# Kernel tuning notes

Hardware: AMD Instinct MI355X
Metric: run time of the kernel (lower is better)

The kernel has to match this reference:

```python
import jax, jax.numpy as jnp
import numpy as np

B, T, D, H = 2, 2048, 1024, 16  # batch, seq_len, d_model (d_in==d_out), num_heads
HD = D // H  # head_dim = 64


def setup_inputs() -> dict:
    key = jax.random.key(0)
    ks = jax.random.split(key, 6)
    s = 1.0 / np.sqrt(D)
    return {
        "x": jax.random.normal(ks[0], (B, T, D), dtype=jnp.float32),
        "wq": jax.random.normal(ks[1], (D, D), dtype=jnp.float32) * s,
        "wk": jax.random.normal(ks[2], (D, D), dtype=jnp.float32) * s,
        "wv": jax.random.normal(ks[3], (D, D), dtype=jnp.float32) * s,
        "wo": jax.random.normal(ks[4], (D, D), dtype=jnp.float32) * s,
        "bo": jax.random.normal(ks[5], (D,), dtype=jnp.float32) * 0.01,
    }


def reference(x, wq, wk, wv, wo, bo):
    b, t, d = x.shape
    # projections (qkv_bias=False), split heads: [b, h, t, hd]
    q = (x @ wq).reshape(b, t, H, HD).transpose(0, 2, 1, 3)
    k = (x @ wk).reshape(b, t, H, HD).transpose(0, 2, 1, 3)
    v = (x @ wv).reshape(b, t, H, HD).transpose(0, 2, 1, 3)
    # causal attention scores [b, h, t, t]
    scores = jnp.einsum("bhqd,bhkd->bhqk", q, k) / jnp.sqrt(jnp.float32(HD))
    causal = jnp.tril(jnp.ones((t, t), dtype=bool))
    scores = jnp.where(causal[None, None, :, :], scores, -jnp.inf)
    attn = jax.nn.softmax(scores, axis=-1)  # dropout p=0.0 -> identity
    ctx = jnp.einsum("bhqk,bhkd->bhqd", attn, v)  # [b, h, t, hd]
    ctx = ctx.transpose(0, 2, 1, 3).reshape(b, t, d)  # merge heads
    return ctx @ wo + bo
```

## Files before the change

### kernel.cpp

```cpp
#include <hip/hip_runtime.h>
#include <hip/hip_bf16.h>
#include <stdint.h>

#define B_  2
#define T_  2048
#define D_  1024
#define H_  16
#define HD_ 64

typedef __bf16 bf16x8 __attribute__((ext_vector_type(8)));
typedef __bf16 bf16x4 __attribute__((ext_vector_type(4)));
typedef float  f32x4  __attribute__((ext_vector_type(4)));

__device__ __forceinline__ void async_copy16(const void* g, void* l) {
  __builtin_amdgcn_global_load_lds((__attribute__((address_space(1))) void*)(g),
                                   (__attribute__((address_space(3))) void*)(l),
                                   16, 0, 0);
}

__global__ void prep_kernel(const float* __restrict__ x,
                            const float* __restrict__ wq, const float* __restrict__ wk,
                            const float* __restrict__ wv, const float* __restrict__ wo,
                            __bf16* __restrict__ xc,
                            __bf16* __restrict__ wqkv_t, __bf16* __restrict__ wo_t) {
  const int id  = blockIdx.x;
  const int tid = threadIdx.x;
  if (id < 4096) {
    __shared__ __bf16 tile[32][33];
    const int z   = id >> 10;
    const int rem = id & 1023;
    const int n0 = (rem & 31) * 32, k0 = (rem >> 5) * 32;
    const int tx = tid & 31, ty = tid >> 5;
    const float* src = (z == 0) ? wq : (z == 1) ? wk : (z == 2) ? wv : wo;
    __bf16* dst = (z < 3) ? (wqkv_t + (size_t)z * 1024 * 1024) : wo_t;
#pragma unroll
    for (int i = 0; i < 4; ++i)
      tile[ty + 8 * i][tx] = (__bf16)src[(size_t)(k0 + ty + 8 * i) * 1024 + n0 + tx];
    __syncthreads();
#pragma unroll
    for (int i = 0; i < 4; ++i)
      dst[(size_t)(n0 + ty + 8 * i) * 1024 + k0 + tx] = tile[tx][ty + 8 * i];
  } else {
    const int i0 = ((id - 4096) * 256 + tid) * 4;
    bf16x4 v;
#pragma unroll
    for (int k = 0; k < 4; ++k) v[k] = (__bf16)x[i0 + k];
    *(bf16x4*)(xc + i0) = v;
  }
}

template <int MODE>
__launch_bounds__(256)
__global__ void gemm128_kernel(const __bf16* __restrict__ A, const __bf16* __restrict__ Bt, int K,
                               __bf16* __restrict__ q_b, __bf16* __restrict__ k_b,
                               __bf16* __restrict__ vt_b,
                               const float* __restrict__ bo, float* __restrict__ outp) {
  __shared__ __align__(16) __bf16 As[128 * 64];
  __shared__ __align__(16) __bf16 Bs[128 * 64];
  const int tid  = threadIdx.x;
  const int w    = tid >> 6, lane = tid & 63;
  const int quad = lane >> 4, lr = lane & 15;
  const int tm = blockIdx.y * 128, tn = blockIdx.x * 128;
  const int wm = (w >> 1) * 64, wn = (w & 1) * 64;
  const int lrow   = lane >> 3;
  const int gchunk = (lane & 7) ^ lrow;

  f32x4 acc[4][4] = {};

  for (int k0 = 0; k0 < K; k0 += 64) {
#pragma unroll
    for (int c = 0; c < 4; ++c) {
      const int chunk = w * 4 + c;
      const int row   = chunk * 8 + lrow;
      async_copy16(A  + (size_t)(tm + row) * K + k0 + gchunk * 8, As + chunk * 512);
      async_copy16(Bt + (size_t)(tn + row) * K + k0 + gchunk * 8, Bs + chunk * 512);
    }
    __syncthreads();
#pragma unroll
    for (int ks = 0; ks < 2; ++ks) {
      bf16x8 af[4], bfr[4];
#pragma unroll
      for (int mi = 0; mi < 4; ++mi) {
        const int row = wm + mi * 16 + lr;
        const int ch  = (ks * 4 + quad) ^ (row & 7);
        af[mi] = *(const bf16x8*)(As + row * 64 + ch * 8);
      }
#pragma unroll
      for (int ni = 0; ni < 4; ++ni) {
        const int row = wn + ni * 16 + lr;
        const int ch  = (ks * 4 + quad) ^ (row & 7);
        bfr[ni] = *(const bf16x8*)(Bs + row * 64 + ch * 8);
      }
#pragma unroll
      for (int mi = 0; mi < 4; ++mi)
#pragma unroll
        for (int ni = 0; ni < 4; ++ni)
          acc[mi][ni] = __builtin_amdgcn_mfma_f32_16x16x32_bf16(af[mi], bfr[ni], acc[mi][ni], 0, 0, 0);
    }
    __syncthreads();
  }

  if (MODE == 0) {
#pragma unroll
    for (int mi = 0; mi < 4; ++mi) {
      const int mrow0 = tm + wm + mi * 16 + quad * 4;
      const int b  = mrow0 >> 11;
      const int t0 = mrow0 & 2047;
#pragma unroll
      for (int ni = 0; ni < 4; ++ni) {
        const int ncol = tn + wn + ni * 16 + lr;
        const int mat  = ncol >> 10;
        const int nn   = ncol & 1023;
        const int h = nn >> 6, hd = nn & 63;
        if (mat == 0) {
#pragma unroll
          for (int r = 0; r < 4; ++r)
            q_b[((size_t)((b * H_ + h) * T_ + t0 + r)) * HD_ + hd] =
                (__bf16)(acc[mi][ni][r] * 0.125f);
        } else if (mat == 1) {
#pragma unroll
          for (int r = 0; r < 4; ++r)
            k_b[((size_t)((b * H_ + h) * T_ + t0 + r)) * HD_ + hd] =
                (__bf16)(acc[mi][ni][r]);
        } else {
          bf16x4 pk;
#pragma unroll
          for (int r = 0; r < 4; ++r) pk[r] = (__bf16)(acc[mi][ni][r]);
          *(bf16x4*)(vt_b + ((size_t)(b * H_ + h) * HD_ + hd) * T_ + t0) = pk;
        }
      }
    }
  } else {
#pragma unroll
    for (int mi = 0; mi < 4; ++mi) {
      const int m0 = tm + wm + mi * 16 + quad * 4;
#pragma unroll
      for (int ni = 0; ni < 4; ++ni) {
        const int n = tn + wn + ni * 16 + lr;
        const float bias = bo[n];
#pragma unroll
        for (int r = 0; r < 4; ++r)
          outp[(size_t)(m0 + r) * D_ + n] = acc[mi][ni][r] + bias;
      }
    }
  }
}

__launch_bounds__(256, 3)
__global__ void attn_kernel(const __bf16* __restrict__ q_b, const __bf16* __restrict__ k_b,
                            const __bf16* __restrict__ vt_b, __bf16* __restrict__ ctx) {
  __shared__ __align__(16) __bf16 sK[64 * 64];
  __shared__ __align__(16) __bf16 sV[64 * 64];
  __shared__ __align__(16) __bf16 sP[2][64][72];
  const int tid  = threadIdx.x;
  const int w    = tid >> 6, lane = tid & 63;
  const int quad = lane >> 4, lr = lane & 15;
  const int id = blockIdx.x;
  const int bh  = (id & 7) * 4 + ((id >> 3) & 3);
  const int t0i = (id >> 5) & 7;
  const int rnd = id >> 8;
  const int tq  = (3 - rnd) * 8 + ((rnd & 1) ? t0i : (7 - t0i));
  const __bf16* qh = q_b  + (size_t)bh * T_ * HD_;
  const __bf16* kh = k_b  + (size_t)bh * T_ * HD_;
  const __bf16* vh = vt_b + (size_t)bh * HD_ * T_;
  const int b = bh >> 4, h = bh & 15;

  const int r0 = tid >> 3, r1 = (tid + 256) >> 3;
  const int g0 = tid & 7;

  const int q0 = tq * 64;
  const int nj = tq + 1;
  const int w16 = w * 16;

  bf16x8 qf[4][2];
#pragma unroll
  for (int qs = 0; qs < 4; ++qs)
#pragma unroll
    for (int ks = 0; ks < 2; ++ks)
      qf[qs][ks] = *(const bf16x8*)(qh + (size_t)(q0 + qs * 16 + lr) * HD_ + ks * 32 + quad * 8);

  bf16x8 onesf;
#pragma unroll
  for (int j = 0; j < 8; ++j) onesf[j] = (__bf16)1.0f;

  f32x4 o[4] = {};
  f32x4 ls = {};

  bf16x8 kr0 = *(const bf16x8*)(kh + (size_t)r0 * HD_ + g0 * 8);
  bf16x8 kr1 = *(const bf16x8*)(kh + (size_t)r1 * HD_ + g0 * 8);
  bf16x8 vr0 = *(const bf16x8*)(vh + (size_t)r0 * T_ + g0 * 8);
  bf16x8 vr1 = *(const bf16x8*)(vh + (size_t)r1 * T_ + g0 * 8);

  for (int j = 0; j < nj; ++j) {
    const int j0 = j * 64;
    const int pb = j & 1;
    __syncthreads();
    *(bf16x8*)(sK + r0 * 64 + (g0 ^ (r0 & 7)) * 8) = kr0;
    *(bf16x8*)(sK + r1 * 64 + (g0 ^ (r1 & 7)) * 8) = kr1;
    *(bf16x8*)(sV + r0 * 64 + (g0 ^ (r0 & 7)) * 8) = vr0;
    *(bf16x8*)(sV + r1 * 64 + (g0 ^ (r1 & 7)) * 8) = vr1;
    __syncthreads();
    if (j + 1 < nj) {
      const int jn = j0 + 64;
      kr0 = *(const bf16x8*)(kh + (size_t)(jn + r0) * HD_ + g0 * 8);
      kr1 = *(const bf16x8*)(kh + (size_t)(jn + r1) * HD_ + g0 * 8);
      vr0 = *(const bf16x8*)(vh + (size_t)r0 * T_ + jn + g0 * 8);
      vr1 = *(const bf16x8*)(vh + (size_t)r1 * T_ + jn + g0 * 8);
    }
    const int krow = w16 + lr;
    bf16x8 kf[2];
    kf[0] = *(const bf16x8*)(sK + krow * 64 + ((quad) ^ (krow & 7)) * 8);
    kf[1] = *(const bf16x8*)(sK + krow * 64 + ((4 + quad) ^ (krow & 7)) * 8);
    f32x4 s[4] = {};
    __builtin_amdgcn_s_setprio(1);
#pragma unroll
    for (int qs = 0; qs < 4; ++qs) {
      s[qs] = __builtin_amdgcn_mfma_f32_16x16x32_bf16(qf[qs][0], kf[0], s[qs], 0, 0, 0);
      s[qs] = __builtin_amdgcn_mfma_f32_16x16x32_bf16(qf[qs][1], kf[1], s[qs], 0, 0, 0);
    }
    __builtin_amdgcn_s_setprio(0);
    if (j0 + 63 > q0) {
      const int col = j0 + w16 + lr;
#pragma unroll
      for (int qs = 0; qs < 4; ++qs)
#pragma unroll
        for (int r = 0; r < 4; ++r) {
          const int row = q0 + qs * 16 + quad * 4 + r;
          if (col > row) s[qs][r] = -3.0e38f;
        }
    }
#pragma unroll
    for (int qs = 0; qs < 4; ++qs)
#pragma unroll
      for (int r = 0; r < 4; ++r)
        s[qs][r] = __expf(s[qs][r]);
#pragma unroll
    for (int qs = 0; qs < 4; ++qs)
#pragma unroll
      for (int r = 0; r < 4; ++r)
        sP[pb][qs * 16 + quad * 4 + r][w16 + lr] = (__bf16)s[qs][r];
    __syncthreads();
    bf16x8 pf[2];
#pragma unroll
    for (int ks = 0; ks < 2; ++ks)
      pf[ks] = *(const bf16x8*)(&sP[pb][w16 + lr][ks * 32 + quad * 8]);
    __builtin_amdgcn_s_setprio(1);
#pragma unroll
    for (int ni = 0; ni < 4; ++ni) {
      const int row = ni * 16 + lr;
#pragma unroll
      for (int ks = 0; ks < 2; ++ks) {
        const int ch = (ks * 4 + quad) ^ (row & 7);
        bf16x8 vf = *(const bf16x8*)(sV + row * 64 + ch * 8);
        o[ni] = __builtin_amdgcn_mfma_f32_16x16x32_bf16(pf[ks], vf, o[ni], 0, 0, 0);
      }
    }
    ls = __builtin_amdgcn_mfma_f32_16x16x32_bf16(pf[0], onesf, ls, 0, 0, 0);
    ls = __builtin_amdgcn_mfma_f32_16x16x32_bf16(pf[1], onesf, ls, 0, 0, 0);
    __builtin_amdgcn_s_setprio(0);
  }
#pragma unroll
  for (int r = 0; r < 4; ++r) {
    const float inv = 1.0f / ls[r];
    const int t = q0 + w16 + quad * 4 + r;
#pragma unroll
    for (int ni = 0; ni < 4; ++ni)
      ctx[((size_t)(b * T_ + t)) * D_ + h * HD_ + ni * 16 + lr] =
          (__bf16)(o[ni][r] * inv);
  }
}

extern "C" void kernel_launch(void* const* d_in, const int* in_sizes, int n_in,
                              void* d_out, int out_size, void* d_ws, size_t ws_size,
                              hipStream_t stream) {
  (void)in_sizes; (void)n_in; (void)out_size; (void)ws_size;
  const float* x  = (const float*)d_in[0];
  const float* wq = (const float*)d_in[1];
  const float* wk = (const float*)d_in[2];
  const float* wv = (const float*)d_in[3];
  const float* wo = (const float*)d_in[4];
  const float* bo = (const float*)d_in[5];
  float* outp = (float*)d_out;

  char* ws = (char*)d_ws;
  __bf16* ctx    = (__bf16*)(ws + 0);
  __bf16* wqkv_t = (__bf16*)(ws + 0);
  __bf16* wo_t   = (__bf16*)(ws + 8388608);
  __bf16* q_b    = (__bf16*)(ws + 10485760);
  __bf16* k_b    = (__bf16*)(ws + 18874368);
  __bf16* vt_b   = (__bf16*)(ws + 27262976);
  __bf16* xc     = (__bf16*)(ws + 35651584);

  prep_kernel<<<8192, 256, 0, stream>>>(x, wq, wk, wv, wo, xc, wqkv_t, wo_t);
  gemm128_kernel<0><<<dim3(24, 32), 256, 0, stream>>>(xc, wqkv_t, 1024, q_b, k_b, vt_b, nullptr, nullptr);
  attn_kernel<<<1024, 256, 0, stream>>>(q_b, k_b, vt_b, ctx);
  gemm128_kernel<1><<<dim3(8, 32), 256, 0, stream>>>(ctx, wo_t, 1024, nullptr, nullptr, nullptr, bo, outp);
}
```

Measured before the change: 176.9 us.

## Replace QKV projection GEMM with 256x256 double-buffered async-pipelined kernel

Adds a dedicated QKV projection kernel that uses 256x256 output tiles, 512 threads, and double-buffered LDS filled by async global-to-LDS copies. Loads for later k-steps are interleaved between four MFMA sub-phases, with explicit barriers, waitcnts and setprio. The goal is to hide global-load latency and raise data reuse per tile compared with the single-buffered 128x128 GEMM. The grid is also remapped for locality, and the x cast now uses a vectorized float4 load. The costs are 128 KB of LDS, heavy register pressure, and hand-written synchronization that could be fragile.

```diff
diff --git a/kernel.cpp b/kernel.cpp
--- a/kernel.cpp
+++ b/kernel.cpp
@@ -17,6 +17,9 @@
                                    (__attribute__((address_space(3))) void*)(l),
                                    16, 0, 0);
 }
+
+#define FENCE() asm volatile("" ::: "memory")
+#define BAR()   do { FENCE(); __builtin_amdgcn_s_barrier(); FENCE(); } while (0)
 
 __global__ void prep_kernel(const float* __restrict__ x,
                             const float* __restrict__ wq, const float* __restrict__ wk,
@@ -42,18 +45,182 @@
       dst[(size_t)(n0 + ty + 8 * i) * 1024 + k0 + tx] = tile[tx][ty + 8 * i];
   } else {
     const int i0 = ((id - 4096) * 256 + tid) * 4;
+    const f32x4 f = *(const f32x4*)(x + i0);
     bf16x4 v;
 #pragma unroll
-    for (int k = 0; k < 4; ++k) v[k] = (__bf16)x[i0 + k];
+    for (int k = 0; k < 4; ++k) v[k] = (__bf16)f[k];
     *(bf16x4*)(xc + i0) = v;
   }
 }
 
-template <int MODE>
+__launch_bounds__(512, 2)
+__global__ void gemm256_kernel(const __bf16* __restrict__ A, const __bf16* __restrict__ Bt,
+                               __bf16* __restrict__ q_b, __bf16* __restrict__ k_b,
+                               __bf16* __restrict__ vt_b) {
+  __shared__ __align__(16) __bf16 As[2][16384];
+  __shared__ __align__(16) __bf16 Bs[2][16384];
+  const int NT = 16;
+
+  const int tid  = threadIdx.x;
+  const int w    = tid >> 6, lane = tid & 63;
+  const int quad = lane >> 4, lr = lane & 15;
+  const int lrow = lane >> 3, g = lane & 7;
+
+  const int orig = blockIdx.x;
+  const int wgid = (orig & 7) * 24 + (orig >> 3);
+  const int by = wgid & 15, bx = wgid >> 4;
+  const int tm = by * 256, tn = bx * 256;
+  const int wm = (w >> 2) * 128, wn = (w & 3) * 64;
+  const int rg0 = w * 2, rg1 = rg0 + 1;
+
+  auto stage = [&](const __bf16* __restrict__ X, int rowbase, __bf16 (*Xs)[16384],
+                   int slot, int h, int kt) {
+    const int k0 = kt * 64;
+    const int co = (g ^ lrow) * 8;
+    async_copy16(X + (size_t)(rowbase + h * 128 + rg0 * 8 + lrow) * 1024 + k0 + co,
+                 &Xs[slot][h * 8192 + rg0 * 512]);
+    async_copy16(X + (size_t)(rowbase + h * 128 + rg1 * 8 + lrow) * 1024 + k0 + co,
+                 &Xs[slot][h * 8192 + rg1 * 512]);
+  };
+
+  f32x4  acc[8][4] = {};
+  bf16x8 afr[4][2], bfr[4][2];
+
+  stage(Bt, tn, Bs, 0, 0, 0);
+  stage(A,  tm, As, 0, 0, 0);
+  stage(Bt, tn, Bs, 0, 1, 0);
+  stage(A,  tm, As, 0, 1, 0);
+  stage(Bt, tn, Bs, 1, 0, 1);
+  stage(A,  tm, As, 1, 0, 1);
+  asm volatile("s_waitcnt vmcnt(4)" ::: "memory");
+  BAR();
+
+  for (int t = 0; t < NT; ++t) {
+    const int cur = t & 1;
+    const int tn1 = (t + 1 < NT) ? (t + 1) : (NT - 1);
+    const int tn2 = (t + 2 < NT) ? (t + 2) : (NT - 1);
+    const int s1 = (t + 1) & 1, s2 = t & 1;
+    const __bf16* Ac = As[cur];
+    const __bf16* Bc = Bs[cur];
+
+#pragma unroll
+    for (int mi = 0; mi < 4; ++mi) {
+      const int row = wm + mi * 16 + lr;
+#pragma unroll
+      for (int ks = 0; ks < 2; ++ks)
+        afr[mi][ks] = *(const bf16x8*)(Ac + row * 64 + (((ks * 4 + quad) ^ (row & 7)) * 8));
+    }
+#pragma unroll
+    for (int ni = 0; ni < 2; ++ni) {
+      const int row = wn + ni * 16 + lr;
+#pragma unroll
+      for (int ks = 0; ks < 2; ++ks)
+        bfr[ni][ks] = *(const bf16x8*)(Bc + row * 64 + (((ks * 4 + quad) ^ (row & 7)) * 8));
+    }
+    stage(Bt, tn, Bs, s1, 1, tn1);
+    BAR();
+    asm volatile("s_waitcnt lgkmcnt(0)" ::: "memory");
+    __builtin_amdgcn_s_setprio(1);
+#pragma unroll
+    for (int mi = 0; mi < 4; ++mi)
+#pragma unroll
+      for (int ni = 0; ni < 2; ++ni)
+#pragma unroll
+        for (int ks = 0; ks < 2; ++ks)
+          acc[mi][ni] = __builtin_amdgcn_mfma_f32_16x16x32_bf16(afr[mi][ks], bfr[ni][ks], acc[mi][ni], 0, 0, 0);
+    __builtin_amdgcn_s_setprio(0);
+    BAR();
+
+#pragma unroll
+    for (int ni = 2; ni < 4; ++ni) {
+      const int row = wn + ni * 16 + lr;
+#pragma unroll
+      for (int ks = 0; ks < 2; ++ks)
+        bfr[ni][ks] = *(const bf16x8*)(Bc + row * 64 + (((ks * 4 + quad) ^ (row & 7)) * 8));
+    }
+    stage(A, tm, As, s1, 1, tn1);
+    BAR();
+    asm volatile("s_waitcnt lgkmcnt(0)" ::: "memory");
+    __builtin_amdgcn_s_setprio(1);
+#pragma unroll
+    for (int mi = 0; mi < 4; ++mi)
+#pragma unroll
+      for (int ni = 2; ni < 4; ++ni)
+#pragma unroll
+        for (int ks = 0; ks < 2; ++ks)
+          acc[mi][ni] = __builtin_amdgcn_mfma_f32_16x16x32_bf16(afr[mi][ks], bfr[ni][ks], acc[mi][ni], 0, 0, 0);
+    __builtin_amdgcn_s_setprio(0);
+    BAR();
+
+#pragma unroll
+    for (int mi = 0; mi < 4; ++mi) {
+      const int row = wm + 64 + mi * 16 + lr;
+#pragma unroll
+      for (int ks = 0; ks < 2; ++ks)
+        afr[mi][ks] = *(const bf16x8*)(Ac + row * 64 + (((ks * 4 + quad) ^ (row & 7)) * 8));
+    }
+    stage(Bt, tn, Bs, s2, 0, tn2);
+    BAR();
+    asm volatile("s_waitcnt lgkmcnt(0)" ::: "memory");
+    __builtin_amdgcn_s_setprio(1);
+#pragma unroll
+    for (int mi = 0; mi < 4; ++mi)
+#pragma unroll
+      for (int ni = 0; ni < 2; ++ni)
+#pragma unroll
+        for (int ks = 0; ks < 2; ++ks)
+          acc[mi + 4][ni] = __builtin_amdgcn_mfma_f32_16x16x32_bf16(afr[mi][ks], bfr[ni][ks], acc[mi + 4][ni], 0, 0, 0);
+    __builtin_amdgcn_s_setprio(0);
+    BAR();
+
+    stage(A, tm, As, s2, 0, tn2);
+    BAR();
+    __builtin_amdgcn_s_setprio(1);
+#pragma unroll
+    for (int mi = 0; mi < 4; ++mi)
+#pragma unroll
+      for (int ni = 2; ni < 4; ++ni)
+#pragma unroll
+        for (int ks = 0; ks < 2; ++ks)
+          acc[mi + 4][ni] = __builtin_amdgcn_mfma_f32_16x16x32_bf16(afr[mi][ks], bfr[ni][ks], acc[mi + 4][ni], 0, 0, 0);
+    __builtin_amdgcn_s_setprio(0);
+    asm volatile("s_waitcnt vmcnt(4)" ::: "memory");
+    BAR();
+  }
+
+#pragma unroll
+  for (int mi = 0; mi < 8; ++mi) {
+    const int mrow0 = tm + wm + mi * 16 + quad * 4;
+    const int b  = mrow0 >> 11;
+    const int t0 = mrow0 & 2047;
+#pragma unroll
+    for (int ni = 0; ni < 4; ++ni) {
+      const int ncol = tn + wn + ni * 16 + lr;
+      const int mat  = ncol >> 10;
+      const int nn   = ncol & 1023;
+      const int h = nn >> 6, hd = nn & 63;
+      if (mat == 0) {
+#pragma unroll
+        for (int r = 0; r < 4; ++r)
+          q_b[((size_t)((b * H_ + h) * T_ + t0 + r)) * HD_ + hd] =
+              (__bf16)(acc[mi][ni][r] * 0.125f);
+      } else if (mat == 1) {
+#pragma unroll
+        for (int r = 0; r < 4; ++r)
+          k_b[((size_t)((b * H_ + h) * T_ + t0 + r)) * HD_ + hd] =
+              (__bf16)(acc[mi][ni][r]);
+      } else {
+        bf16x4 pk;
+#pragma unroll
+        for (int r = 0; r < 4; ++r) pk[r] = (__bf16)(acc[mi][ni][r]);
+        *(bf16x4*)(vt_b + ((size_t)(b * H_ + h) * HD_ + hd) * T_ + t0) = pk;
+      }
+    }
+  }
+}
+
 __launch_bounds__(256)
 __global__ void gemm128_kernel(const __bf16* __restrict__ A, const __bf16* __restrict__ Bt, int K,
-                               __bf16* __restrict__ q_b, __bf16* __restrict__ k_b,
-                               __bf16* __restrict__ vt_b,
                                const float* __restrict__ bo, float* __restrict__ outp) {
   __shared__ __align__(16) __bf16 As[128 * 64];
   __shared__ __align__(16) __bf16 Bs[128 * 64];
@@ -100,48 +267,16 @@
     __syncthreads();
   }
 
-  if (MODE == 0) {
-#pragma unroll
-    for (int mi = 0; mi < 4; ++mi) {
-      const int mrow0 = tm + wm + mi * 16 + quad * 4;
-      const int b  = mrow0 >> 11;
-      const int t0 = mrow0 & 2047;
-#pragma unroll
-      for (int ni = 0; ni < 4; ++ni) {
-        const int ncol = tn + wn + ni * 16 + lr;
-        const int mat  = ncol >> 10;
-        const int nn   = ncol & 1023;
-        const int h = nn >> 6, hd = nn & 63;
-        if (mat == 0) {
-#pragma unroll
-          for (int r = 0; r < 4; ++r)
-            q_b[((size_t)((b * H_ + h) * T_ + t0 + r)) * HD_ + hd] =
-                (__bf16)(acc[mi][ni][r] * 0.125f);
-        } else if (mat == 1) {
-#pragma unroll
-          for (int r = 0; r < 4; ++r)
-            k_b[((size_t)((b * H_ + h) * T_ + t0 + r)) * HD_ + hd] =
-                (__bf16)(acc[mi][ni][r]);
-        } else {
-          bf16x4 pk;
-#pragma unroll
-          for (int r = 0; r < 4; ++r) pk[r] = (__bf16)(acc[mi][ni][r]);
-          *(bf16x4*)(vt_b + ((size_t)(b * H_ + h) * HD_ + hd) * T_ + t0) = pk;
-        }
-      }
-    }
-  } else {
-#pragma unroll
-    for (int mi = 0; mi < 4; ++mi) {
-      const int m0 = tm + wm + mi * 16 + quad * 4;
-#pragma unroll
-      for (int ni = 0; ni < 4; ++ni) {
-        const int n = tn + wn + ni * 16 + lr;
-        const float bias = bo[n];
-#pragma unroll
-        for (int r = 0; r < 4; ++r)
-          outp[(size_t)(m0 + r) * D_ + n] = acc[mi][ni][r] + bias;
-      }
+#pragma unroll
+  for (int mi = 0; mi < 4; ++mi) {
+    const int m0 = tm + wm + mi * 16 + quad * 4;
+#pragma unroll
+    for (int ni = 0; ni < 4; ++ni) {
+      const int n = tn + wn + ni * 16 + lr;
+      const float bias = bo[n];
+#pragma unroll
+      for (int r = 0; r < 4; ++r)
+        outp[(size_t)(m0 + r) * D_ + n] = acc[mi][ni][r] + bias;
     }
   }
 }
@@ -292,7 +427,7 @@
   __bf16* xc     = (__bf16*)(ws + 35651584);
 
   prep_kernel<<<8192, 256, 0, stream>>>(x, wq, wk, wv, wo, xc, wqkv_t, wo_t);
-  gemm128_kernel<0><<<dim3(24, 32), 256, 0, stream>>>(xc, wqkv_t, 1024, q_b, k_b, vt_b, nullptr, nullptr);
+  gemm256_kernel<<<192, 512, 0, stream>>>(xc, wqkv_t, q_b, k_b, vt_b);
   attn_kernel<<<1024, 256, 0, stream>>>(q_b, k_b, vt_b, ctx);
-  gemm128_kernel<1><<<dim3(8, 32), 256, 0, stream>>>(ctx, wo_t, 1024, nullptr, nullptr, nullptr, bo, outp);
-}
+  gemm128_kernel<<<dim3(8, 32), 256, 0, stream>>>(ctx, wo_t, 1024, bo, outp);
+}
```

Result: slower. 188.3 us (+6.4%).
